# Performance work log

Measured on AMD Instinct MI355X. Metric: run time of the kernel, lower is better.

The kernel has to match this reference:

```python
import jax, jax.numpy as jnp
import numpy as np

B, T, D, H = 16, 4096, 1024, 32
EPS = 1e-6


def setup_inputs() -> dict:
    key = jax.random.key(0)
    ks = jax.random.split(key, 12)
    inp = {
        'Z_real': jax.random.normal(ks[0], (B, T, D), jnp.float32),
        'Z_imag': jax.random.normal(ks[1], (B, T, D), jnp.float32),
        'mask': jnp.ones((B, T), jnp.float32),
        # psi_mag: Linear(1,H) -> GELU -> Linear(H,1)  (xavier gain 0.1, zero bias)
        'W1m': jax.random.normal(ks[2], (H, 1), jnp.float32) * 0.1,
        'b1m': jnp.zeros((H,), jnp.float32),
        'W2m': jax.random.normal(ks[3], (1, H), jnp.float32) * 0.1,
        'b2m': jnp.zeros((1,), jnp.float32),
        # psi_phase: Linear(2,H) -> GELU -> Linear(H,2)
        'W1p': jax.random.normal(ks[4], (H, 2), jnp.float32) * 0.1,
        'b1p': jnp.zeros((H,), jnp.float32),
        'W2p': jax.random.normal(ks[5], (2, H), jnp.float32) * 0.1,
        'b2p': jnp.zeros((2,), jnp.float32),
        'mag_scale': jnp.float32(0.1),
    }
    return inp


def reference(Z_real, Z_imag, mask, W1m, b1m, W2m, b2m, W1p, b1p, W2p, b2p, mag_scale):
    m = mask[:, :, None]  # (B,T,1)
    count = jnp.clip(jnp.sum(m, axis=1, keepdims=True), 1.0)  # (B,1,1)
    Ar = jnp.sum(Z_real * m, axis=1, keepdims=True) / count   # (B,1,D)
    Ai = jnp.sum(Z_imag * m, axis=1, keepdims=True) / count
    mag = jnp.sqrt(Ar * Ar + Ai * Ai)
    log_mag = jnp.log(mag + EPS)                               # (B,1,D)
    phase_vec = jnp.stack([Ar, Ai], axis=-1) / (mag[..., None] + EPS)  # (B,1,D,2)
    # psi_mag on scalar feature
    h = jax.nn.gelu(log_mag[..., None] @ W1m.T + b1m, approximate=False)  # (B,1,D,H)
    mag_delta = (h @ W2m.T + b2m)[..., 0]                      # (B,1,D)
    log_mag_out = log_mag + mag_scale * mag_delta
    # psi_phase on 2-vector
    hp = jax.nn.gelu(phase_vec @ W1p.T + b1p, approximate=False)  # (B,1,D,H)
    pv = hp @ W2p.T + b2p                                      # (B,1,D,2)
    norm = jnp.maximum(jnp.sqrt(jnp.sum(pv * pv, axis=-1, keepdims=True)), 1e-12)
    pv = pv / norm
    r_out = jnp.exp(log_mag_out)
    A_new_r = r_out * pv[..., 0]
    A_new_i = r_out * pv[..., 1]
    out = jnp.stack([Z_real + A_new_r, Z_imag + A_new_i], axis=0)  # (2,B,T,D)
    return out
```

## Files before the change

kernel.cpp:

```cpp
#include <hip/hip_runtime.h>
#include <math.h>

#define BB 16
#define TT 4096
#define DD 1024
#define HH 32
#define TCHUNK 64
#define NCHUNK (TT / TCHUNK)

static constexpr float kEPS = 1e-6f;

typedef float f32x4 __attribute__((ext_vector_type(4)));

__global__ __launch_bounds__(256) void reduce_kernel(
    const float* __restrict__ zr, const float* __restrict__ zi,
    const float* __restrict__ mask,
    float* __restrict__ partR, float* __restrict__ partI,
    float* __restrict__ cntP) {
  const int c = blockIdx.x;
  const int b = blockIdx.y;
  const int tid = threadIdx.x;
  const int d4 = tid * 4;

  f32x4 accR = (f32x4)(0.f);
  f32x4 accI = (f32x4)(0.f);
  float msum = 0.f;

  const size_t base = ((size_t)b * TT + (size_t)c * TCHUNK) * DD + d4;
  const float* zrp = zr + base;
  const float* zip = zi + base;
  const float* mp = mask + (size_t)b * TT + (size_t)c * TCHUNK;

  #pragma unroll 8
  for (int t = 0; t < TCHUNK; ++t) {
    const float m = mp[t];
    msum += m;
    f32x4 r  = *(const f32x4*)(zrp + (size_t)t * DD);
    f32x4 im = *(const f32x4*)(zip + (size_t)t * DD);
    accR += r * m;
    accI += im * m;
  }

  const size_t po = ((size_t)c * BB + b) * DD + d4;
  *(f32x4*)(partR + po) = accR;
  *(f32x4*)(partI + po) = accI;
  if (tid == 0) cntP[c * BB + b] = msum;
}

__global__ __launch_bounds__(256) void mlp_kernel(
    const float* __restrict__ partR, const float* __restrict__ partI,
    const float* __restrict__ cntP,
    const float* __restrict__ W1m, const float* __restrict__ b1m,
    const float* __restrict__ W2m, const float* __restrict__ b2m,
    const float* __restrict__ W1p, const float* __restrict__ b1p,
    const float* __restrict__ W2p, const float* __restrict__ b2p,
    const float* __restrict__ mag_scale,
    float* __restrict__ anR, float* __restrict__ anI) {
  const int i = blockIdx.x * blockDim.x + threadIdx.x;
  const int b = i >> 10;
  const int d = i & (DD - 1);

  __shared__ float cntS;
  if (threadIdx.x == 0) {
    float s = 0.f;
    for (int c = 0; c < NCHUNK; ++c) s += cntP[c * BB + b];
    cntS = s;
  }
  __syncthreads();

  float sR = 0.f, sI = 0.f;
  for (int c = 0; c < NCHUNK; ++c) {
    const size_t po = ((size_t)c * BB + b) * DD + d;
    sR += partR[po];
    sI += partI[po];
  }

  const float count = fmaxf(cntS, 1.0f);
  const float Ar = sR / count;
  const float Ai = sI / count;
  const float mag = sqrtf(Ar * Ar + Ai * Ai);
  const float log_mag = logf(mag + kEPS);
  const float inv_me = 1.0f / (mag + kEPS);
  const float pr = Ar * inv_me;
  const float pi = Ai * inv_me;

  float md = b2m[0];
  #pragma unroll
  for (int j = 0; j < HH; ++j) {
    float h = log_mag * W1m[j] + b1m[j];
    h = 0.5f * h * (1.0f + erff(h * 0.70710678118654752440f));
    md += h * W2m[j];
  }
  const float lmo = log_mag + mag_scale[0] * md;

  float pv0 = b2p[0];
  float pv1 = b2p[1];
  #pragma unroll
  for (int j = 0; j < HH; ++j) {
    float hp = pr * W1p[2 * j] + pi * W1p[2 * j + 1] + b1p[j];
    hp = 0.5f * hp * (1.0f + erff(hp * 0.70710678118654752440f));
    pv0 += hp * W2p[j];
    pv1 += hp * W2p[HH + j];
  }
  const float nrm = fmaxf(sqrtf(pv0 * pv0 + pv1 * pv1), 1e-12f);
  const float r_out = expf(lmo);
  anR[i] = r_out * pv0 / nrm;
  anI[i] = r_out * pv1 / nrm;
}

__global__ __launch_bounds__(256) void add_kernel(
    const float* __restrict__ zr, const float* __restrict__ zi,
    const float* __restrict__ anR, const float* __restrict__ anI,
    float* __restrict__ out) {
  const int c = blockIdx.x;
  const int b = blockIdx.y;
  const int tid = threadIdx.x;
  const int d4 = tid * 4;

  const int o = b * DD + d4;
  const f32x4 ar4 = *(const f32x4*)(anR + o);
  const f32x4 ai4 = *(const f32x4*)(anI + o);

  const size_t base = ((size_t)b * TT + (size_t)c * TCHUNK) * DD + d4;
  const float* zrp = zr + base;
  const float* zip = zi + base;
  float* out0 = out + base;
  float* out1 = out + (size_t)BB * TT * DD + base;

  #pragma unroll 8
  for (int t = TCHUNK - 1; t >= 0; --t) {
    const size_t ro = (size_t)t * DD;
    f32x4 r  = __builtin_nontemporal_load((const f32x4*)(zrp + ro));
    f32x4 im = __builtin_nontemporal_load((const f32x4*)(zip + ro));
    r += ar4;
    im += ai4;
    __builtin_nontemporal_store(r, (f32x4*)(out0 + ro));
    __builtin_nontemporal_store(im, (f32x4*)(out1 + ro));
  }
}

extern "C" void kernel_launch(void* const* d_in, const int* in_sizes, int n_in,
                              void* d_out, int out_size, void* d_ws, size_t ws_size,
                              hipStream_t stream) {
  const float* zr = (const float*)d_in[0];
  const float* zi = (const float*)d_in[1];
  const float* mask = (const float*)d_in[2];
  const float* W1m = (const float*)d_in[3];
  const float* b1m = (const float*)d_in[4];
  const float* W2m = (const float*)d_in[5];
  const float* b2m = (const float*)d_in[6];
  const float* W1p = (const float*)d_in[7];
  const float* b1p = (const float*)d_in[8];
  const float* W2p = (const float*)d_in[9];
  const float* b2p = (const float*)d_in[10];
  const float* mag_scale = (const float*)d_in[11];

  float* ws = (float*)d_ws;
  float* partR = ws;
  float* partI = ws + 1048576;
  float* cntP  = ws + 2097152;
  float* anR   = ws + 2098176;
  float* anI   = ws + 2114560;

  dim3 g(NCHUNK, BB);
  reduce_kernel<<<g, 256, 0, stream>>>(zr, zi, mask, partR, partI, cntP);

  mlp_kernel<<<BB * DD / 256, 256, 0, stream>>>(
      partR, partI, cntP, W1m, b1m, W2m, b2m, W1p, b1p, W2p, b2p, mag_scale, anR, anI);

  add_kernel<<<g, 256, 0, stream>>>(zr, zi, anR, anI, (float*)d_out);
}
```

Before: 282.7 us.

## Process batches in groups of four so Z stays cached between reduce and add

```diff
diff --git a/kernel.cpp b/kernel.cpp
--- a/kernel.cpp
+++ b/kernel.cpp
@@ -5,8 +5,10 @@
 #define TT 4096
 #define DD 1024
 #define HH 32
-#define TCHUNK 64
-#define NCHUNK (TT / TCHUNK)
+#define GROUPB 4
+#define NGROUP (BB / GROUPB)
+#define RCHUNK 16
+#define NCH (TT / RCHUNK)
 
 static constexpr float kEPS = 1e-6f;
 
@@ -16,9 +18,10 @@
     const float* __restrict__ zr, const float* __restrict__ zi,
     const float* __restrict__ mask,
     float* __restrict__ partR, float* __restrict__ partI,
-    float* __restrict__ cntP) {
+    float* __restrict__ cntP, int gbase) {
   const int c = blockIdx.x;
-  const int b = blockIdx.y;
+  const int gb = blockIdx.y;
+  const int b = gbase + gb;
   const int tid = threadIdx.x;
   const int d4 = tid * 4;
 
@@ -26,13 +29,13 @@
   f32x4 accI = (f32x4)(0.f);
   float msum = 0.f;
 
-  const size_t base = ((size_t)b * TT + (size_t)c * TCHUNK) * DD + d4;
+  const size_t base = ((size_t)b * TT + (size_t)c * RCHUNK) * DD + d4;
   const float* zrp = zr + base;
   const float* zip = zi + base;
-  const float* mp = mask + (size_t)b * TT + (size_t)c * TCHUNK;
+  const float* mp = mask + (size_t)b * TT + (size_t)c * RCHUNK;
 
-  #pragma unroll 8
-  for (int t = 0; t < TCHUNK; ++t) {
+  #pragma unroll
+  for (int t = 0; t < RCHUNK; ++t) {
     const float m = mp[t];
     msum += m;
     f32x4 r  = *(const f32x4*)(zrp + (size_t)t * DD);
@@ -41,10 +44,10 @@
     accI += im * m;
   }
 
-  const size_t po = ((size_t)c * BB + b) * DD + d4;
+  const size_t po = ((size_t)(gb * NCH + c)) * DD + d4;
   *(f32x4*)(partR + po) = accR;
   *(f32x4*)(partI + po) = accI;
-  if (tid == 0) cntP[c * BB + b] = msum;
+  if (tid == 0) cntP[gb * NCH + c] = msum;
 }
 
 __global__ __launch_bounds__(256) void mlp_kernel(
@@ -56,26 +59,27 @@
     const float* __restrict__ W2p, const float* __restrict__ b2p,
     const float* __restrict__ mag_scale,
     float* __restrict__ anR, float* __restrict__ anI) {
-  const int i = blockIdx.x * blockDim.x + threadIdx.x;
-  const int b = i >> 10;
-  const int d = i & (DD - 1);
+  const int gid = blockIdx.x * blockDim.x + threadIdx.x;
+  const int gb = gid >> 10;
+  const int d = gid & (DD - 1);
 
-  __shared__ float cntS;
-  if (threadIdx.x == 0) {
-    float s = 0.f;
-    for (int c = 0; c < NCHUNK; ++c) s += cntP[c * BB + b];
-    cntS = s;
+  __shared__ float red[256];
+  red[threadIdx.x] = cntP[gb * NCH + threadIdx.x];
+  __syncthreads();
+  for (int s = 128; s > 0; s >>= 1) {
+    if (threadIdx.x < s) red[threadIdx.x] += red[threadIdx.x + s];
+    __syncthreads();
   }
-  __syncthreads();
+  const float count = fmaxf(red[0], 1.0f);
 
   float sR = 0.f, sI = 0.f;
-  for (int c = 0; c < NCHUNK; ++c) {
-    const size_t po = ((size_t)c * BB + b) * DD + d;
+  #pragma unroll 8
+  for (int c = 0; c < NCH; ++c) {
+    const size_t po = ((size_t)(gb * NCH + c)) * DD + d;
     sR += partR[po];
     sI += partI[po];
   }
 
-  const float count = fmaxf(cntS, 1.0f);
   const float Ar = sR / count;
   const float Ai = sI / count;
   const float mag = sqrtf(Ar * Ar + Ai * Ai);
@@ -104,34 +108,35 @@
   }
   const float nrm = fmaxf(sqrtf(pv0 * pv0 + pv1 * pv1), 1e-12f);
   const float r_out = expf(lmo);
-  anR[i] = r_out * pv0 / nrm;
-  anI[i] = r_out * pv1 / nrm;
+  anR[gid] = r_out * pv0 / nrm;
+  anI[gid] = r_out * pv1 / nrm;
 }
 
 __global__ __launch_bounds__(256) void add_kernel(
     const float* __restrict__ zr, const float* __restrict__ zi,
     const float* __restrict__ anR, const float* __restrict__ anI,
-    float* __restrict__ out) {
+    float* __restrict__ out, int gbase) {
   const int c = blockIdx.x;
-  const int b = blockIdx.y;
+  const int gb = blockIdx.y;
+  const int b = gbase + gb;
   const int tid = threadIdx.x;
   const int d4 = tid * 4;
 
-  const int o = b * DD + d4;
+  const int o = gb * DD + d4;
   const f32x4 ar4 = *(const f32x4*)(anR + o);
   const f32x4 ai4 = *(const f32x4*)(anI + o);
 
-  const size_t base = ((size_t)b * TT + (size_t)c * TCHUNK) * DD + d4;
+  const size_t base = ((size_t)b * TT + (size_t)c * RCHUNK) * DD + d4;
   const float* zrp = zr + base;
   const float* zip = zi + base;
   float* out0 = out + base;
   float* out1 = out + (size_t)BB * TT * DD + base;
 
-  #pragma unroll 8
-  for (int t = TCHUNK - 1; t >= 0; --t) {
+  #pragma unroll
+  for (int t = 0; t < RCHUNK; ++t) {
     const size_t ro = (size_t)t * DD;
-    f32x4 r  = __builtin_nontemporal_load((const f32x4*)(zrp + ro));
-    f32x4 im = __builtin_nontemporal_load((const f32x4*)(zip + ro));
+    f32x4 r  = *(const f32x4*)(zrp + ro);
+    f32x4 im = *(const f32x4*)(zip + ro);
     r += ar4;
     im += ai4;
     __builtin_nontemporal_store(r, (f32x4*)(out0 + ro));
@@ -160,13 +165,15 @@
   float* partI = ws + 1048576;
   float* cntP  = ws + 2097152;
   float* anR   = ws + 2098176;
-  float* anI   = ws + 2114560;
+  float* anI   = ws + 2102272;
 
-  dim3 g(NCHUNK, BB);
-  reduce_kernel<<<g, 256, 0, stream>>>(zr, zi, mask, partR, partI, cntP);
-
-  mlp_kernel<<<BB * DD / 256, 256, 0, stream>>>(
-      partR, partI, cntP, W1m, b1m, W2m, b2m, W1p, b1p, W2p, b2p, mag_scale, anR, anI);
-
-  add_kernel<<<g, 256, 0, stream>>>(zr, zi, anR, anI, (float*)d_out);
+  dim3 g(NCH, GROUPB);
+  for (int grp = 0; grp < NGROUP; ++grp) {
+    const int gbase = grp * GROUPB;
+    reduce_kernel<<<g, 256, 0, stream>>>(zr, zi, mask, partR, partI, cntP, gbase);
+    mlp_kernel<<<GROUPB * DD / 256, 256, 0, stream>>>(
+        partR, partI, cntP, W1m, b1m, W2m, b2m, W1p, b1p, W2p, b2p, mag_scale,
+        anR, anI);
+    add_kernel<<<g, 256, 0, stream>>>(zr, zi, anR, anI, (float*)d_out, gbase);
+  }
 }
```

After: 414.3 us. +46.6%, slower.
